# Kernel tuning notes

Hardware: AMD Instinct MI355X
Metric: run time of the kernel (lower is better)

The kernel has to match this reference:

```python
import jax, jax.numpy as jnp
import numpy as np

FP8_E4M3_MAX = 448.0
FP4_E2M1_MAX = 6.0
BLOCK = 16  # NVFP4 block-scale granularity


def _round_e4m3(x):
    """Round non-negative values to fp8 e4m3 grid (3 mantissa bits, min normal 2^-6, max 448)."""
    a = jnp.abs(x)
    e = jnp.clip(jnp.floor(jnp.log2(jnp.where(a > 0, a, 1.0))), -6.0, 8.0)
    s = jnp.exp2(e)
    q = jnp.round(a / s * 8.0) / 8.0 * s
    q = jnp.clip(q, 0.0, FP8_E4M3_MAX)
    return jnp.where(a > 0, q, 0.0)


def _round_e2m1(x):
    """Round to fp4 e2m1 grid: +/- {0, 0.5, 1, 1.5, 2, 3, 4, 6}."""
    sgn = jnp.sign(x)
    a = jnp.clip(jnp.abs(x), 0.0, FP4_E2M1_MAX)
    e = jnp.clip(jnp.floor(jnp.log2(jnp.where(a > 0, a, 1.0))), 0.0, 2.0)
    step = jnp.exp2(e) * 0.5  # 0.5 in [0,2), 1 in [2,4), 2 in [4,6]
    q = jnp.round(a / step) * step
    return sgn * jnp.clip(q, 0.0, FP4_E2M1_MAX)


def quant_nvfp4(t):
    """Dynamic NVFP4 quantization (vLLM scaled_fp4_quant semantics).
    Returns (q_fp4 [R, K/16, 16], block_scale_e4m3 [R, K/16], global_scale []).
    Dequant: q * block_scale / global_scale."""
    gs = (FP8_E4M3_MAX * FP4_E2M1_MAX) / jnp.max(jnp.abs(t))
    tb = t.reshape(t.shape[0], -1, BLOCK)
    block_amax = jnp.max(jnp.abs(tb), axis=-1)              # [R, K/16]
    bs = _round_e4m3(block_amax / FP4_E2M1_MAX * gs)         # e4m3 block scales
    safe_bs = jnp.where(bs > 0, bs, 1.0)
    q = _round_e2m1(tb * (gs / safe_bs)[..., None])
    q = jnp.where((bs > 0)[..., None], q, 0.0)
    return q, bs, gs


def setup_inputs() -> dict:
    key = jax.random.key(0)
    kx, kw = jax.random.split(key)
    tokens, hidden = 8192, 4096
    x = jax.random.normal(kx, (tokens, 2 * hidden), dtype=jnp.float32)
    w = jax.random.uniform(kw, (hidden, hidden), dtype=jnp.float32)
    return {"x": x, "w": w}


def reference(x, w):
    d = x.shape[-1] // 2
    # SiluAndMul
    y = jax.nn.silu(x[..., :d]) * x[..., d:]                # [T, H]
    # dynamic NVFP4 quant of activation and weight
    qy, sy, gy = quant_nvfp4(y)
    qw, sw, gw = quant_nvfp4(w)
    # cutlass_scaled_fp4_mm: out = (qy*sy) @ (qw*sw)^T * alpha, alpha = 1/(gy*gw)
    a = (qy * sy[..., None]).reshape(y.shape)               # [T, H]
    b = (qw * sw[..., None]).reshape(w.shape)               # [H, H]
    alpha = 1.0 / (gy * gw)
    return (a @ b.T) * alpha
```

## Files before the change

### kernel.cpp

```cpp
#include <hip/hip_runtime.h>
#include <hip/hip_bf16.h>

typedef __attribute__((ext_vector_type(8))) short bf16x8;
typedef __attribute__((ext_vector_type(4))) float f32x4;


__device__ __forceinline__ float silu_mul_f(float a, float b) {
  float s = 1.0f / (1.0f + expf(-a));
  return (a * s) * b;
}

__device__ __forceinline__ int flog2(float a) {
  return (int)((__float_as_uint(a) >> 23) & 255u) - 127;
}
__device__ __forceinline__ float exp2i(int e) {
  return __uint_as_float((unsigned)(e + 127) << 23);
}

__device__ __forceinline__ float round_e4m3_f(float a) {
  if (!(a > 0.0f)) return 0.0f;
  int e = flog2(a);
  e = e < -6 ? -6 : (e > 8 ? 8 : e);
  float q = rintf(a * exp2i(3 - e)) * exp2i(e - 3);
  return fminf(q, 448.0f);
}

__device__ __forceinline__ float round_e2m1_f(float x) {
  float a = fminf(fabsf(x), 6.0f);
  if (!(a > 0.0f)) return 0.0f;
  int e = flog2(a);
  e = e < 0 ? 0 : (e > 2 ? 2 : e);
  float q = rintf(a * exp2i(1 - e)) * exp2i(e - 1);
  q = fminf(q, 6.0f);
  return (x < 0.0f) ? -q : q;
}

__global__ void init_scal_kernel(float* scal) {
  if (threadIdx.x < 2) scal[threadIdx.x] = 0.0f;
}


__device__ __forceinline__ float act_unit_max(const float* __restrict__ x, long u,
                                              int hidden, long hqm, int hqLog) {
  long row = u >> hqLog, c = u & hqm;
  const float* xr = x + ((row * (long)hidden) << 1);
  float4 v1 = ((const float4*)xr)[c];
  float4 v2 = ((const float4*)(xr + hidden))[c];
  float m = fmaxf(fabsf(silu_mul_f(v1.x, v2.x)), fabsf(silu_mul_f(v1.y, v2.y)));
  m = fmaxf(m, fmaxf(fabsf(silu_mul_f(v1.z, v2.z)), fabsf(silu_mul_f(v1.w, v2.w))));
  return m;
}

__global__ void amax2_kernel(const float* __restrict__ x, const float* __restrict__ w,
                             float* __restrict__ scal, long actU, long wU,
                             int hidden, int hqLog, int AB) {
  const long hqm = (1L << hqLog) - 1;
  float m = 0.0f;
  int which;
  if ((int)blockIdx.x < AB) {
    which = 0;
    const long stride = (long)AB * blockDim.x;
    long u = (long)blockIdx.x * blockDim.x + threadIdx.x;
    for (; u + stride < actU; u += 2 * stride) {
      float m0 = act_unit_max(x, u, hidden, hqm, hqLog);
      float m1 = act_unit_max(x, u + stride, hidden, hqm, hqLog);
      m = fmaxf(m, fmaxf(m0, m1));
    }
    if (u < actU) m = fmaxf(m, act_unit_max(x, u, hidden, hqm, hqLog));
  } else {
    which = 1;
    const long stride = (long)(gridDim.x - AB) * blockDim.x;
    long u = (long)((int)blockIdx.x - AB) * blockDim.x + threadIdx.x;
    for (; u + stride < wU; u += 2 * stride) {
      float4 v1 = ((const float4*)w)[u];
      float4 v2 = ((const float4*)w)[u + stride];
      float m0 = fmaxf(fmaxf(fabsf(v1.x), fabsf(v1.y)), fmaxf(fabsf(v1.z), fabsf(v1.w)));
      float m1 = fmaxf(fmaxf(fabsf(v2.x), fabsf(v2.y)), fmaxf(fabsf(v2.z), fabsf(v2.w)));
      m = fmaxf(m, fmaxf(m0, m1));
    }
    if (u < wU) {
      float4 v = ((const float4*)w)[u];
      m = fmaxf(m, fmaxf(fmaxf(fabsf(v.x), fabsf(v.y)), fmaxf(fabsf(v.z), fabsf(v.w))));
    }
  }
#pragma unroll
  for (int off = 32; off > 0; off >>= 1) m = fmaxf(m, __shfl_xor(m, off));
  __shared__ float sm[4];
  if ((threadIdx.x & 63) == 0) sm[threadIdx.x >> 6] = m;
  __syncthreads();
  if (threadIdx.x == 0) {
    float mm = fmaxf(fmaxf(sm[0], sm[1]), fmaxf(sm[2], sm[3]));
    atomicMax((unsigned int*)(scal + which), __float_as_uint(mm));
  }
}


__device__ __forceinline__ void quant_unit(float y0, float y1, float y2, float y3,
                                           float gs, unsigned short* dst) {
  float lm = fmaxf(fmaxf(fabsf(y0), fabsf(y1)), fmaxf(fabsf(y2), fabsf(y3)));
  lm = fmaxf(lm, __shfl_xor(lm, 1));
  lm = fmaxf(lm, __shfl_xor(lm, 2));
  float bs = round_e4m3_f(lm / 6.0f * gs);
  float r = gs / (bs > 0.0f ? bs : 1.0f);
  ushort4 o;
  o.x = (unsigned short)(__float_as_uint(round_e2m1_f(y0 * r) * bs) >> 16);
  o.y = (unsigned short)(__float_as_uint(round_e2m1_f(y1 * r) * bs) >> 16);
  o.z = (unsigned short)(__float_as_uint(round_e2m1_f(y2 * r) * bs) >> 16);
  o.w = (unsigned short)(__float_as_uint(round_e2m1_f(y3 * r) * bs) >> 16);
  *(ushort4*)dst = o;
}

__global__ void quant2_kernel(const float* __restrict__ x, const float* __restrict__ w,
                              __hip_bfloat16* __restrict__ A, __hip_bfloat16* __restrict__ B,
                              const float* __restrict__ scal, long actU, long wU,
                              int hidden, int hqLog, int AB) {
  const long hqm = (1L << hqLog) - 1;
  if ((int)blockIdx.x < AB) {
    const float gs = 2688.0f / scal[0];
    const long stride = (long)AB * blockDim.x;
    long u = (long)blockIdx.x * blockDim.x + threadIdx.x;
    for (; u + stride < actU; u += 2 * stride) {
      long ua = u, ub = u + stride;
      long ra = ua >> hqLog, ca = ua & hqm;
      long rb = ub >> hqLog, cb = ub & hqm;
      const float* xa = x + ((ra * (long)hidden) << 1) + (ca << 2);
      const float* xb = x + ((rb * (long)hidden) << 1) + (cb << 2);
      float4 a1 = *(const float4*)xa;
      float4 a2 = *(const float4*)(xa + hidden);
      float4 b1 = *(const float4*)xb;
      float4 b2 = *(const float4*)(xb + hidden);
      quant_unit(silu_mul_f(a1.x, a2.x), silu_mul_f(a1.y, a2.y),
                 silu_mul_f(a1.z, a2.z), silu_mul_f(a1.w, a2.w),
                 gs, (unsigned short*)A + (ua << 2));
      quant_unit(silu_mul_f(b1.x, b2.x), silu_mul_f(b1.y, b2.y),
                 silu_mul_f(b1.z, b2.z), silu_mul_f(b1.w, b2.w),
                 gs, (unsigned short*)A + (ub << 2));
    }
    if (u < actU) {
      long c = u & hqm;
      const float* xa = x + (((u >> hqLog) * (long)hidden) << 1) + (c << 2);
      float4 v1 = *(const float4*)xa;
      float4 v2 = *(const float4*)(xa + hidden);
      quant_unit(silu_mul_f(v1.x, v2.x), silu_mul_f(v1.y, v2.y),
                 silu_mul_f(v1.z, v2.z), silu_mul_f(v1.w, v2.w),
                 gs, (unsigned short*)A + (u << 2));
    }
  } else {
    const float gs = 2688.0f / scal[1];
    const long stride = (long)(gridDim.x - AB) * blockDim.x;
    long u = (long)((int)blockIdx.x - AB) * blockDim.x + threadIdx.x;
    for (; u + stride < wU; u += 2 * stride) {
      float4 v1 = ((const float4*)w)[u];
      float4 v2 = ((const float4*)w)[u + stride];
      quant_unit(v1.x, v1.y, v1.z, v1.w, gs, (unsigned short*)B + (u << 2));
      quant_unit(v2.x, v2.y, v2.z, v2.w, gs, (unsigned short*)B + ((u + stride) << 2));
    }
    if (u < wU) {
      float4 v = ((const float4*)w)[u];
      quant_unit(v.x, v.y, v.z, v.w, gs, (unsigned short*)B + (u << 2));
    }
  }
}


__device__ __forceinline__ void gload_lds16(const void* g, void* l) {
  __builtin_amdgcn_global_load_lds(
      (const __attribute__((address_space(1))) void*)(uintptr_t)g,
      (__attribute__((address_space(3))) void*)(uintptr_t)l, 16, 0, 0);
}

template <unsigned IMM>
__device__ __forceinline__ bf16x8 lds_read16o(unsigned addr) {
  bf16x8 r;
  asm volatile("ds_read_b128 %0, %1 offset:%c2" : "=&v"(r) : "v"(addr), "i"(IMM));
  return r;
}

__device__ __forceinline__ f32x4 mfma_(bf16x8 a, bf16x8 b, f32x4 c) {
  return __builtin_amdgcn_mfma_f32_16x16x32_bf16(a, b, c, 0, 0, 0);
}

#define SP1 __builtin_amdgcn_s_setprio(1)
#define SP0 __builtin_amdgcn_s_setprio(0)
#define SCHEDB __builtin_amdgcn_sched_barrier(0)
#define WAITL(n) do { asm volatile("s_waitcnt lgkmcnt(" #n ")" ::: "memory"); SCHEDB; } while (0)
#define VMW4 do { asm volatile("s_waitcnt vmcnt(4)" ::: "memory"); } while (0)

#define STAGEA(PP, HH, KSB) do {                                        \
    const char* _s = pa + (KSB) + (HH) * 64;                            \
    gload_lds16(_s, ldsStA + (PP) * 32768 + (HH) * 16384);              \
    gload_lds16(_s + rowBig, ldsStA + (PP) * 32768 + (HH) * 16384 + 8192); } while (0)

#define STAGEB(PP, HH, KSB) do {                                        \
    const char* _s = pb + (KSB) + (HH) * 64;                            \
    gload_lds16(_s, ldsStB + (PP) * 32768 + (HH) * 16384);              \
    gload_lds16(_s + rowBig, ldsStB + (PP) * 32768 + (HH) * 16384 + 8192); } while (0)

#define RDA4(DST, PP, HH, MB) do {                                              \
    DST[0] = lds_read16o<(PP)*32768u + (HH)*16384u + ((MB)+0)*1024u>(vA);       \
    DST[1] = lds_read16o<(PP)*32768u + (HH)*16384u + ((MB)+1)*1024u>(vA);       \
    DST[2] = lds_read16o<(PP)*32768u + (HH)*16384u + ((MB)+2)*1024u>(vA);       \
    DST[3] = lds_read16o<(PP)*32768u + (HH)*16384u + ((MB)+3)*1024u>(vA); } while (0)

#define RDB4(DST, PP, HH) do {                                                  \
    DST[0] = lds_read16o<(PP)*32768u + (HH)*16384u + 0u>(vB);                   \
    DST[1] = lds_read16o<(PP)*32768u + (HH)*16384u + 1024u>(vB);                \
    DST[2] = lds_read16o<(PP)*32768u + (HH)*16384u + 2048u>(vB);                \
    DST[3] = lds_read16o<(PP)*32768u + (HH)*16384u + 3072u>(vB); } while (0)

#define MFMA16(AF, BF, MB) do {                                                  \
    acc[(MB)+0][0] = mfma_(AF[0], BF[0], acc[(MB)+0][0]);                        \
    acc[(MB)+1][0] = mfma_(AF[1], BF[0], acc[(MB)+1][0]);                        \
    acc[(MB)+2][0] = mfma_(AF[2], BF[0], acc[(MB)+2][0]);                        \
    acc[(MB)+3][0] = mfma_(AF[3], BF[0], acc[(MB)+3][0]);                        \
    acc[(MB)+0][1] = mfma_(AF[0], BF[1], acc[(MB)+0][1]);                        \
    acc[(MB)+1][1] = mfma_(AF[1], BF[1], acc[(MB)+1][1]);                        \
    acc[(MB)+2][1] = mfma_(AF[2], BF[1], acc[(MB)+2][1]);                        \
    acc[(MB)+3][1] = mfma_(AF[3], BF[1], acc[(MB)+3][1]);                        \
    acc[(MB)+0][2] = mfma_(AF[0], BF[2], acc[(MB)+0][2]);                        \
    acc[(MB)+1][2] = mfma_(AF[1], BF[2], acc[(MB)+1][2]);                        \
    acc[(MB)+2][2] = mfma_(AF[2], BF[2], acc[(MB)+2][2]);                        \
    acc[(MB)+3][2] = mfma_(AF[3], BF[2], acc[(MB)+3][2]);                        \
    acc[(MB)+0][3] = mfma_(AF[0], BF[3], acc[(MB)+0][3]);                        \
    acc[(MB)+1][3] = mfma_(AF[1], BF[3], acc[(MB)+1][3]);                        \
    acc[(MB)+2][3] = mfma_(AF[2], BF[3], acc[(MB)+2][3]);                        \
    acc[(MB)+3][3] = mfma_(AF[3], BF[3], acc[(MB)+3][3]); } while (0)

#define TILE(P, KSB) do {                                                        \
    STAGEA((P)^1, 0, KSB);                                                       \
    RDA4(aY, P, 0, 4);                                                           \
    SP1; WAITL(4);                                                               \
    MFMA16(aX, bb0, 0); SP0;                                                     \
    STAGEB((P)^1, 0, KSB);                                                       \
    VMW4;                                                                        \
    __builtin_amdgcn_s_barrier(); SCHEDB;                                        \
    RDA4(aX, P, 1, 0); RDB4(bb1, P, 1);                                          \
    SP1; WAITL(8);                                                               \
    MFMA16(aY, bb0, 4); SP0;                                                     \
    STAGEA((P)^1, 1, KSB);                                                       \
    RDA4(aY, P, 1, 4);                                                           \
    SP1; WAITL(4);                                                               \
    MFMA16(aX, bb1, 0); SP0;                                                     \
    STAGEB((P)^1, 1, KSB);                                                       \
    WAITL(0);                                                                    \
    VMW4;                                                                        \
    __builtin_amdgcn_s_barrier(); SCHEDB;                                        \
    RDA4(aX, (P)^1, 0, 0); RDB4(bb0, (P)^1, 0); SCHEDB;                          \
    SP1; MFMA16(aY, bb1, 4); SP0;                                                \
  } while (0)

__global__ __launch_bounds__(512, 2) void gemm_bt_kernel(
    const __hip_bfloat16* __restrict__ A, const __hip_bfloat16* __restrict__ B,
    float* __restrict__ C, const float* __restrict__ scal, int M, int N, int K) {
  __shared__ __align__(16) char lds[131072];

  const int nbm = M >> 8, nbn = N >> 8;
  int wg = blockIdx.x, bm, bn;
  if ((nbm & 7) == 0) {
    int band = nbm >> 3;
    int xcd = wg & 7, c = wg >> 3;
    bm = xcd * band + (c % band);
    bn = c / band;
  } else {
    bm = wg / nbn; bn = wg % nbn;
  }
  const int brow = bm << 8, bcol = bn << 8;

  const int tid = threadIdx.x;
  const int lane = tid & 63;
  const int wave = tid >> 6;
  const int wm = wave >> 2, wn = wave & 3;

  const int srow = tid >> 2;
  const int slc = (tid & 3) ^ ((tid >> 3) & 3);
  const char* pa = (const char*)(A + (size_t)(brow + srow) * K + slc * 8);
  const char* pb = (const char*)(B + (size_t)(bcol + srow) * K + slc * 8);
  const size_t rowBig = (size_t)128 * K * 2;
  char* ldsStA = lds + tid * 16;
  char* ldsStB = lds + 65536 + tid * 16;

  const unsigned ldsBase = (unsigned)(uintptr_t)lds;
  const unsigned xoff = (unsigned)((lane & 15) * 64) +
                        ((((unsigned)(lane >> 4)) ^ (((unsigned)lane >> 1) & 3u)) << 4);
  const unsigned vA = ldsBase + (unsigned)(wm * 8192) + xoff;
  const unsigned vB = ldsBase + 65536u + (unsigned)(wn * 4096) + xoff;

  f32x4 acc[8][4] = {};
  bf16x8 aX[4], aY[4], bb0[4], bb1[4];

  STAGEA(0, 0, 0); STAGEB(0, 0, 0); STAGEA(0, 1, 0); STAGEB(0, 1, 0);
  asm volatile("s_waitcnt vmcnt(0)" ::: "memory");
  __syncthreads();
  RDA4(aX, 0, 0, 0); RDB4(bb0, 0, 0); SCHEDB;

  const int nt = K >> 6;
  for (int it = 0; it < (nt >> 1); ++it) {
    int t0 = it << 1;
    int ks0 = (t0 + 1) * 128;
    int ks1 = (t0 + 2 == nt) ? 0 : (t0 + 2) * 128;
    TILE(0, ks0);
    TILE(1, ks1);
  }
  asm volatile("s_waitcnt lgkmcnt(0)" ::: "memory");
  asm volatile("s_waitcnt vmcnt(0)" ::: "memory");

  float gy = 2688.0f / scal[0];
  float gw = 2688.0f / scal[1];
  float alpha = 1.0f / (gy * gw);

#pragma unroll
  for (int m = 0; m < 8; ++m) {
    int rbase = brow + wm * 128 + m * 16 + ((lane >> 4) << 2);
#pragma unroll
    for (int n = 0; n < 4; ++n) {
      int col = bcol + wn * 64 + n * 16 + (lane & 15);
#pragma unroll
      for (int rg = 0; rg < 4; ++rg) {
        C[(size_t)(rbase + rg) * N + col] = acc[m][n][rg] * alpha;
      }
    }
  }
}


extern "C" void kernel_launch(void* const* d_in, const int* in_sizes, int n_in,
                              void* d_out, int out_size, void* d_ws, size_t ws_size,
                              hipStream_t stream) {
  const float* x = (const float*)d_in[0];
  const float* w = (const float*)d_in[1];
  float* out = (float*)d_out;

  int hidden = 1;
  while ((long long)hidden * hidden < (long long)in_sizes[1]) hidden <<= 1;
  int tokens = in_sizes[0] / (2 * hidden);

  char* ws = (char*)d_ws;
  __hip_bfloat16* Aq = (__hip_bfloat16*)ws;
  __hip_bfloat16* Bq = (__hip_bfloat16*)(ws + (size_t)tokens * hidden * 2);
  float* scal = (float*)(ws + (size_t)tokens * hidden * 2 + (size_t)hidden * hidden * 2);

  long actU = (long)tokens * hidden / 4;
  long wU = (long)hidden * hidden / 4;
  int hqLog = __builtin_ctz((unsigned)(hidden >> 2));
  int nBlk = 2048;
  int AB = (int)(((long)nBlk * actU) / (actU + wU));
  AB &= ~3;
  if (AB < 1) AB = 1;
  if (AB > nBlk - 1) AB = nBlk - 1;

  init_scal_kernel<<<1, 64, 0, stream>>>(scal);
  amax2_kernel<<<nBlk, 256, 0, stream>>>(x, w, scal, actU, wU, hidden, hqLog, AB);
  quant2_kernel<<<nBlk, 256, 0, stream>>>(x, w, Aq, Bq, scal, actU, wU, hidden, hqLog, AB);

  int grid = (tokens >> 8) * (hidden >> 8);
  gemm_bt_kernel<<<grid, 512, 0, stream>>>(Aq, Bq, out, scal, tokens, hidden, hidden);
}
```

Measured before the change: 387.0 us.

## Shrink GEMM block tile from 256x256 to 128x128 with higher occupancy

The bf16 GEMM block tile drops from 256x256 to 128x128 and LDS use halves to 64KB. Launch bounds now request 4 blocks per CU, and each wave holds a 4x2 accumulator set instead of 8x4. The staging, LDS read and MFMA macros and the vmcnt waits are reworked to match. This trades less data reuse per tile, so more global and LDS traffic per FLOP, for more resident blocks and a larger grid, giving better latency hiding and better load balance across CUs.

```diff
diff --git a/kernel.cpp b/kernel.cpp
--- a/kernel.cpp
+++ b/kernel.cpp
@@ -184,77 +184,54 @@
 #define SP0 __builtin_amdgcn_s_setprio(0)
 #define SCHEDB __builtin_amdgcn_sched_barrier(0)
 #define WAITL(n) do { asm volatile("s_waitcnt lgkmcnt(" #n ")" ::: "memory"); SCHEDB; } while (0)
-#define VMW4 do { asm volatile("s_waitcnt vmcnt(4)" ::: "memory"); } while (0)
-
-#define STAGEA(PP, HH, KSB) do {                                        \
-    const char* _s = pa + (KSB) + (HH) * 64;                            \
-    gload_lds16(_s, ldsStA + (PP) * 32768 + (HH) * 16384);              \
-    gload_lds16(_s + rowBig, ldsStA + (PP) * 32768 + (HH) * 16384 + 8192); } while (0)
-
-#define STAGEB(PP, HH, KSB) do {                                        \
-    const char* _s = pb + (KSB) + (HH) * 64;                            \
-    gload_lds16(_s, ldsStB + (PP) * 32768 + (HH) * 16384);              \
-    gload_lds16(_s + rowBig, ldsStB + (PP) * 32768 + (HH) * 16384 + 8192); } while (0)
-
-#define RDA4(DST, PP, HH, MB) do {                                              \
-    DST[0] = lds_read16o<(PP)*32768u + (HH)*16384u + ((MB)+0)*1024u>(vA);       \
-    DST[1] = lds_read16o<(PP)*32768u + (HH)*16384u + ((MB)+1)*1024u>(vA);       \
-    DST[2] = lds_read16o<(PP)*32768u + (HH)*16384u + ((MB)+2)*1024u>(vA);       \
-    DST[3] = lds_read16o<(PP)*32768u + (HH)*16384u + ((MB)+3)*1024u>(vA); } while (0)
-
-#define RDB4(DST, PP, HH) do {                                                  \
-    DST[0] = lds_read16o<(PP)*32768u + (HH)*16384u + 0u>(vB);                   \
-    DST[1] = lds_read16o<(PP)*32768u + (HH)*16384u + 1024u>(vB);                \
-    DST[2] = lds_read16o<(PP)*32768u + (HH)*16384u + 2048u>(vB);                \
-    DST[3] = lds_read16o<(PP)*32768u + (HH)*16384u + 3072u>(vB); } while (0)
-
-#define MFMA16(AF, BF, MB) do {                                                  \
-    acc[(MB)+0][0] = mfma_(AF[0], BF[0], acc[(MB)+0][0]);                        \
-    acc[(MB)+1][0] = mfma_(AF[1], BF[0], acc[(MB)+1][0]);                        \
-    acc[(MB)+2][0] = mfma_(AF[2], BF[0], acc[(MB)+2][0]);                        \
-    acc[(MB)+3][0] = mfma_(AF[3], BF[0], acc[(MB)+3][0]);                        \
-    acc[(MB)+0][1] = mfma_(AF[0], BF[1], acc[(MB)+0][1]);                        \
-    acc[(MB)+1][1] = mfma_(AF[1], BF[1], acc[(MB)+1][1]);                        \
-    acc[(MB)+2][1] = mfma_(AF[2], BF[1], acc[(MB)+2][1]);                        \
-    acc[(MB)+3][1] = mfma_(AF[3], BF[1], acc[(MB)+3][1]);                        \
-    acc[(MB)+0][2] = mfma_(AF[0], BF[2], acc[(MB)+0][2]);                        \
-    acc[(MB)+1][2] = mfma_(AF[1], BF[2], acc[(MB)+1][2]);                        \
-    acc[(MB)+2][2] = mfma_(AF[2], BF[2], acc[(MB)+2][2]);                        \
-    acc[(MB)+3][2] = mfma_(AF[3], BF[2], acc[(MB)+3][2]);                        \
-    acc[(MB)+0][3] = mfma_(AF[0], BF[3], acc[(MB)+0][3]);                        \
-    acc[(MB)+1][3] = mfma_(AF[1], BF[3], acc[(MB)+1][3]);                        \
-    acc[(MB)+2][3] = mfma_(AF[2], BF[3], acc[(MB)+2][3]);                        \
-    acc[(MB)+3][3] = mfma_(AF[3], BF[3], acc[(MB)+3][3]); } while (0)
-
-#define TILE(P, KSB) do {                                                        \
-    STAGEA((P)^1, 0, KSB);                                                       \
-    RDA4(aY, P, 0, 4);                                                           \
-    SP1; WAITL(4);                                                               \
-    MFMA16(aX, bb0, 0); SP0;                                                     \
-    STAGEB((P)^1, 0, KSB);                                                       \
-    VMW4;                                                                        \
-    __builtin_amdgcn_s_barrier(); SCHEDB;                                        \
-    RDA4(aX, P, 1, 0); RDB4(bb1, P, 1);                                          \
-    SP1; WAITL(8);                                                               \
-    MFMA16(aY, bb0, 4); SP0;                                                     \
-    STAGEA((P)^1, 1, KSB);                                                       \
-    RDA4(aY, P, 1, 4);                                                           \
-    SP1; WAITL(4);                                                               \
-    MFMA16(aX, bb1, 0); SP0;                                                     \
-    STAGEB((P)^1, 1, KSB);                                                       \
-    WAITL(0);                                                                    \
-    VMW4;                                                                        \
-    __builtin_amdgcn_s_barrier(); SCHEDB;                                        \
-    RDA4(aX, (P)^1, 0, 0); RDB4(bb0, (P)^1, 0); SCHEDB;                          \
-    SP1; MFMA16(aY, bb1, 4); SP0;                                                \
+#define VMW2 do { asm volatile("s_waitcnt vmcnt(2)" ::: "memory"); } while (0)
+
+#define STAGEA(PP, HH, KSB) \
+    gload_lds16(pa + (KSB) + (HH) * 64, ldsStA + (PP) * 16384 + (HH) * 8192)
+#define STAGEB(PP, HH, KSB) \
+    gload_lds16(pb + (KSB) + (HH) * 64, ldsStB + (PP) * 16384 + (HH) * 8192)
+
+#define RD2A(DST, PP, HH, MB) do {                                              \
+    DST[0] = lds_read16o<(PP)*16384u + (HH)*8192u + ((MB)+0)*1024u>(vA);        \
+    DST[1] = lds_read16o<(PP)*16384u + (HH)*8192u + ((MB)+1)*1024u>(vA); } while (0)
+
+#define RD2B(DST, PP, HH) do {                                                  \
+    DST[0] = lds_read16o<(PP)*16384u + (HH)*8192u + 0u>(vB);                    \
+    DST[1] = lds_read16o<(PP)*16384u + (HH)*8192u + 1024u>(vB); } while (0)
+
+#define MFMA4(AF, BF, MB) do {                                                  \
+    acc[(MB)+0][0] = mfma_(AF[0], BF[0], acc[(MB)+0][0]);                       \
+    acc[(MB)+1][0] = mfma_(AF[1], BF[0], acc[(MB)+1][0]);                       \
+    acc[(MB)+0][1] = mfma_(AF[0], BF[1], acc[(MB)+0][1]);                       \
+    acc[(MB)+1][1] = mfma_(AF[1], BF[1], acc[(MB)+1][1]); } while (0)
+
+#define TILE(P, KSB) do {                                                       \
+                                                             \
+    STAGEA((P)^1, 0, KSB);                                                      \
+    RD2A(aN, P, 0, 2);                                      \
+    SP1; WAITL(2); MFMA4(aC, bC, 0); SP0;                                       \
+                                                             \
+    STAGEB((P)^1, 0, KSB);                                                      \
+    VMW2; __builtin_amdgcn_s_barrier(); SCHEDB;                                 \
+    RD2A(aC, P, 1, 0); RD2B(bN, P, 1);                  \
+    SP1; WAITL(4); MFMA4(aN, bC, 2); SP0;                                       \
+                                                             \
+    STAGEA((P)^1, 1, KSB);                                                      \
+    RD2A(aN, P, 1, 2);                                     \
+    SP1; WAITL(2); MFMA4(aC, bN, 0); SP0;                                       \
+                                                             \
+    STAGEB((P)^1, 1, KSB);                                                      \
+    VMW2; __builtin_amdgcn_s_barrier(); SCHEDB;                                 \
+    RD2A(aC, (P)^1, 0, 0); RD2B(bC, (P)^1, 0);            \
+    SP1; WAITL(4); MFMA4(aN, bN, 2); SP0;                                       \
   } while (0)
 
-__global__ __launch_bounds__(512, 2) void gemm_bt_kernel(
+__global__ __launch_bounds__(512, 4) void gemm_bt_kernel(
     const __hip_bfloat16* __restrict__ A, const __hip_bfloat16* __restrict__ B,
     float* __restrict__ C, const float* __restrict__ scal, int M, int N, int K) {
-  __shared__ __align__(16) char lds[131072];
-
-  const int nbm = M >> 8, nbn = N >> 8;
+  __shared__ __align__(16) char lds[65536];
+
+  const int nbm = M >> 7, nbn = N >> 7;
   int wg = blockIdx.x, bm, bn;
   if ((nbm & 7) == 0) {
     int band = nbm >> 3;
@@ -264,7 +241,7 @@
   } else {
     bm = wg / nbn; bn = wg % nbn;
   }
-  const int brow = bm << 8, bcol = bn << 8;
+  const int brow = bm << 7, bcol = bn << 7;
 
   const int tid = threadIdx.x;
   const int lane = tid & 63;
@@ -275,23 +252,22 @@
   const int slc = (tid & 3) ^ ((tid >> 3) & 3);
   const char* pa = (const char*)(A + (size_t)(brow + srow) * K + slc * 8);
   const char* pb = (const char*)(B + (size_t)(bcol + srow) * K + slc * 8);
-  const size_t rowBig = (size_t)128 * K * 2;
   char* ldsStA = lds + tid * 16;
-  char* ldsStB = lds + 65536 + tid * 16;
+  char* ldsStB = lds + 32768 + tid * 16;
 
   const unsigned ldsBase = (unsigned)(uintptr_t)lds;
   const unsigned xoff = (unsigned)((lane & 15) * 64) +
                         ((((unsigned)(lane >> 4)) ^ (((unsigned)lane >> 1) & 3u)) << 4);
-  const unsigned vA = ldsBase + (unsigned)(wm * 8192) + xoff;
-  const unsigned vB = ldsBase + 65536u + (unsigned)(wn * 4096) + xoff;
-
-  f32x4 acc[8][4] = {};
-  bf16x8 aX[4], aY[4], bb0[4], bb1[4];
+  const unsigned vA = ldsBase + (unsigned)(wm * 4096) + xoff;
+  const unsigned vB = ldsBase + 32768u + (unsigned)(wn * 2048) + xoff;
+
+  f32x4 acc[4][2] = {};
+  bf16x8 aC[2], aN[2], bC[2], bN[2];
 
   STAGEA(0, 0, 0); STAGEB(0, 0, 0); STAGEA(0, 1, 0); STAGEB(0, 1, 0);
   asm volatile("s_waitcnt vmcnt(0)" ::: "memory");
   __syncthreads();
-  RDA4(aX, 0, 0, 0); RDB4(bb0, 0, 0); SCHEDB;
+  RD2A(aC, 0, 0, 0); RD2B(bC, 0, 0); SCHEDB;
 
   const int nt = K >> 6;
   for (int it = 0; it < (nt >> 1); ++it) {
@@ -309,11 +285,11 @@
   float alpha = 1.0f / (gy * gw);
 
 #pragma unroll
-  for (int m = 0; m < 8; ++m) {
-    int rbase = brow + wm * 128 + m * 16 + ((lane >> 4) << 2);
+  for (int m = 0; m < 4; ++m) {
+    int rbase = brow + wm * 64 + m * 16 + ((lane >> 4) << 2);
 #pragma unroll
-    for (int n = 0; n < 4; ++n) {
-      int col = bcol + wn * 64 + n * 16 + (lane & 15);
+    for (int n = 0; n < 2; ++n) {
+      int col = bcol + wn * 32 + n * 16 + (lane & 15);
 #pragma unroll
       for (int rg = 0; rg < 4; ++rg) {
         C[(size_t)(rbase + rg) * N + col] = acc[m][n][rg] * alpha;
@@ -352,6 +328,6 @@
   amax2_kernel<<<nBlk, 256, 0, stream>>>(x, w, scal, actU, wU, hidden, hqLog, AB);
   quant2_kernel<<<nBlk, 256, 0, stream>>>(x, w, Aq, Bq, scal, actU, wU, hidden, hqLog, AB);
 
-  int grid = (tokens >> 8) * (hidden >> 8);
+  int grid = (tokens >> 7) * (hidden >> 7);
   gemm_bt_kernel<<<grid, 512, 0, stream>>>(Aq, Bq, out, scal, tokens, hidden, hidden);
 }
```

New measurement: 486.2 us. 25.6% more time.
